# Kernel tuning notes

Hardware: AMD Instinct MI355X
Metric: run time of the kernel (lower is better)

Reference implementation:

```python
import jax, jax.numpy as jnp
import numpy as np
import math

# ---- static config (matches init_kwargs) ----
MUL = 16                       # multiplicity of 0e and 1o irreps in/out
IN_DIM = 4 * MUL               # 16x0e + 16x1o -> 16 + 48 = 64 channels
DIAMETER = 7.0
RADIUS = DIAMETER / 2.0
NRB = 8                        # num_radial_basis
STEPS = (1.0, 1.0, 1.0)
N_PATHS = 5                    # 0x0->0, 1x1->0, 0x1->1, 1x0->1, 1x1->1
WEIGHT_NUMEL = N_PATHS * MUL * MUL  # 1280


def _lattice():
    axes = []
    for st in STEPS:
        s = math.floor(RADIUS / st)
        axes.append(np.arange(-s, s + 1.0) * st)
    return np.stack(np.meshgrid(*axes, indexing='ij'), axis=-1).astype(np.float32)  # [kx,ky,kz,3]


def _radial_emb(r):
    # e3nn soft_one_hot_linspace, basis='smooth_finite', cutoff=True
    values = np.linspace(0.0, RADIUS, NRB + 2)[1:-1].astype(np.float32)
    step = values[1] - values[0]
    diff = (r[..., None] - values) / step
    def u(t):  # soft unit step: exp(-1/t) for t>0 else 0
        return np.where(t > 0.0, np.exp(-1.0 / np.where(t > 0.0, t, 1.0)), 0.0)
    return (1.14136 * math.e ** 2 * u(diff + 1.0) * u(1.0 - diff)).astype(np.float32)


def _spherical_harmonics(lat):
    # normalize=True, normalization='component': Y0 = 1, Y1 = sqrt(3) * unit_vec
    n = np.linalg.norm(lat, axis=-1, keepdims=True)
    unit = np.where(n > 0, lat / np.where(n > 0, n, 1.0), 0.0)
    return np.ones(lat.shape[:-1], np.float32), (math.sqrt(3.0) * unit).astype(np.float32)


_LAT = _lattice()
_EMB = jnp.asarray(_radial_emb(np.linalg.norm(_LAT, axis=-1)))  # [kx,ky,kz,NRB]
_sh0_np, _sh1_np = _spherical_harmonics(_LAT)
_SH0, _SH1 = jnp.asarray(_sh0_np), jnp.asarray(_sh1_np)
_eps_np = np.zeros((3, 3, 3), np.float32)
for _i, _j, _k in [(0, 1, 2), (1, 2, 0), (2, 0, 1)]:
    _eps_np[_i, _j, _k] = 1.0
    _eps_np[_i, _k, _j] = -1.0
_EPS = jnp.asarray(_eps_np)


def _build_kernel(tp_weight):
    """Radial-basis matmul + CG tensor-product -> conv kernel [out,in,kx,ky,kz]."""
    kx, ky, kz = _LAT.shape[:3]
    nk = kx * ky * kz
    w = jnp.einsum('xyzb,bn->xyzn', _EMB, tp_weight) / nk
    w = w.reshape(kx, ky, kz, N_PATHS, MUL, MUL)
    w1, w2, w3, w4, w5 = [w[..., p, :, :] for p in range(N_PATHS)]
    # e3nn path weights ('component' norm, 'element' path norm): sqrt(dim_out / fan_in)
    a0 = math.sqrt(1.0 / (2 * MUL))  # -> 0e: paths 1,2 each mul1*mul2 = MUL
    a1 = math.sqrt(3.0 / (3 * MUL))  # -> 1o: paths 3,4,5
    c1 = a0                          # w3j(0,0,0) = 1
    c2 = a0 / math.sqrt(3.0)         # w3j(1,1,0) = delta/sqrt(3)
    c3 = a1 / math.sqrt(3.0)         # w3j(0,1,1) = delta/sqrt(3)
    c4 = a1 / math.sqrt(3.0)         # w3j(1,0,1) = delta/sqrt(3)
    c5 = a1 / math.sqrt(6.0)         # w3j(1,1,1) = eps/sqrt(6)
    Kss = c1 * _SH0[..., None, None] * w1                                  # [k,u,o]
    Kvs = c2 * jnp.einsum('xyzi,xyzuo->xyzuio', _SH1, w2)                  # [k,u,3,o]
    Ksv = c3 * jnp.einsum('xyzk,xyzuo->xyzuok', _SH1, w3)                  # [k,u,o,3]
    eye3 = jnp.eye(3, dtype=w.dtype)
    Kvv = (c4 * jnp.einsum('xyz,ik,xyzuo->xyzuiok', _SH0, eye3, w4)
           + c5 * jnp.einsum('ijk,xyzj,xyzuo->xyzuiok', _EPS, _SH1, w5))   # [k,u,3,o,3]
    top = jnp.concatenate([Kss, Ksv.reshape(kx, ky, kz, MUL, 3 * MUL)], axis=-1)
    bot = jnp.concatenate([Kvs.reshape(kx, ky, kz, 3 * MUL, MUL),
                           Kvv.reshape(kx, ky, kz, 3 * MUL, 3 * MUL)], axis=-1)
    K = jnp.concatenate([top, bot], axis=-2)                               # [kx,ky,kz,in,out]
    return jnp.transpose(K, (4, 3, 0, 1, 2))                               # oixyz


def setup_inputs() -> dict:
    key = jax.random.key(0)
    k1, k2, k3, k4 = jax.random.split(key, 4)
    x = jax.random.normal(k1, (2, IN_DIM, 40, 40, 40), jnp.float32)
    sc_w0 = jax.random.normal(k2, (MUL, MUL), jnp.float32)
    sc_w1 = jax.random.normal(k3, (MUL, MUL), jnp.float32)
    tp_weight = jax.random.normal(k4, (NRB, WEIGHT_NUMEL), jnp.float32)
    return {"x": x, "sc_w0": sc_w0, "sc_w1": sc_w1, "tp_weight": tp_weight}


def reference(x, sc_w0, sc_w1, tp_weight):
    B = x.shape[0]
    sp = x.shape[2:]
    inv = 1.0 / math.sqrt(MUL)  # e3nn Linear fan-in normalization
    x0 = x[:, :MUL]                                  # [B,MUL,D,H,W]
    x1 = x[:, MUL:].reshape(B, MUL, 3, *sp)          # [B,MUL,3,D,H,W]
    sc0 = jnp.einsum('uo,budhw->bodhw', sc_w0, x0) * inv
    sc1 = jnp.einsum('uo,buidhw->boidhw', sc_w1, x1) * inv
    sc = jnp.concatenate([sc0, sc1.reshape(B, 3 * MUL, *sp)], axis=1)
    K = _build_kernel(tp_weight)
    pad = [(s // 2, s // 2) for s in K.shape[2:]]
    conv = jax.lax.conv_general_dilated(
        x, K, window_strides=(1, 1, 1), padding=pad,
        dimension_numbers=('NCDHW', 'OIDHW', 'NCDHW'))
    return sc + conv
```

## Files before the change

kernel.cpp:

```cpp
#include <hip/hip_runtime.h>
#include <stdint.h>


#define NT_REAL 179
#define NT_PAD  180
#define NPAIR   90

#define XCH  1557376
#define XCHB ((size_t)XCH * 2)

#define HBYTES 50176
#define SEGB   12288
#define NSEG   15

typedef short s16x8 __attribute__((ext_vector_type(8)));
typedef float f32x4 __attribute__((ext_vector_type(4)));
typedef float f32x16 __attribute__((ext_vector_type(16)));

struct Taps {
  int n;
  short dl16[NT_PAD];
  unsigned char dz[NT_PAD], dy[NT_PAD], dx[NT_PAD];
};
constexpr Taps mk_taps() {
  Taps t{};
  t.n = 0;
  for (int a = 0; a < 7; ++a)
    for (int b = 0; b < 7; ++b)
      for (int c = 0; c < 7; ++c) {
        int d2 = (a-3)*(a-3) + (b-3)*(b-3) + (c-3)*(c-3);
        if (d2 <= 12) {
          t.dz[t.n] = (unsigned char)a; t.dy[t.n] = (unsigned char)b;
          t.dx[t.n] = (unsigned char)c;
          t.dl16[t.n] = (short)((a*14 + b)*16 + c);
          ++t.n;
        }
      }
  for (int i = t.n; i < NT_PAD; ++i) {
    t.dz[i] = 3; t.dy[i] = 3; t.dx[i] = 3; t.dl16[i] = t.dl16[0];
  }
  return t;
}
__device__ constexpr Taps TAPS = mk_taps();
static_assert(mk_taps().n == NT_REAL, "tap count");

struct DL2 { unsigned int v[NPAIR]; };
constexpr DL2 mk_dl2() {
  DL2 d{};
  Taps t = mk_taps();
  for (int p = 0; p < NPAIR; ++p)
    d.v[p] = (unsigned int)(unsigned short)t.dl16[2*p]
           | ((unsigned int)(unsigned short)t.dl16[2*p + 1] << 16);
  return d;
}
__device__ constexpr DL2 DL2V = mk_dl2();

static __device__ inline unsigned short f2bf(float f) {
  unsigned int u = __float_as_uint(f);
  unsigned int r = u + 0x7FFFu + ((u >> 16) & 1u);
  return (unsigned short)(r >> 16);
}

__device__ __forceinline__ void gl_lds16(const void* g, void* s) {
  __builtin_amdgcn_global_load_lds(
      (const __attribute__((address_space(1))) void*)g,
      (__attribute__((address_space(3))) void*)s, 16, 0, 0);
}

__global__ void prep(const float* __restrict__ x, const float* __restrict__ scw0,
                     const float* __restrict__ scw1, const float* __restrict__ tpw,
                     unsigned short* __restrict__ Xp, unsigned short* __restrict__ Bwp) {
  __shared__ float buf[160 * 65];
  int tid = threadIdx.x;

  if (blockIdx.x < 800) {
    int blk = blockIdx.x;
    int ys = blk % 10; int t2 = blk / 10; int iz = t2 % 40; int b = t2 / 40;
    int y0 = ys * 4;
    const float* src = x + (size_t)b * 4096000 + (size_t)iz * 1600 + (size_t)y0 * 40;
    for (int e = tid; e < 64 * 160; e += 256) {
      int ch = e / 160, i = e - ch * 160;
      buf[i * 65 + ch] = src[(size_t)ch * 64000 + i];
    }
    __syncthreads();
    for (int f = tid; f < 160 * 8; f += 256) {
      int i = f >> 3, g = f & 7;
      int yy = i / 40, xx = i - yy * 40;
      s16x8 v;
      #pragma unroll
      for (int j = 0; j < 8; ++j) v[j] = (short)f2bf(buf[i * 65 + g * 8 + j]);
      size_t pos = ((size_t)((b * 46 + iz + 3) * 46 + (y0 + yy + 3)) * 46 + (xx + 3));
      *reinterpret_cast<s16x8*>(Xp + (size_t)g * XCH + pos * 8) = v;
    }
    return;
  }

  int t = blockIdx.x - 800;
  float (*wsm)[16][16] = reinterpret_cast<float (*)[16][16]>(buf);

  int dz = TAPS.dz[t], dy = TAPS.dy[t], dx = TAPS.dx[t];
  float fz = dz - 3.0f, fy = dy - 3.0f, fx = dx - 3.0f;
  float d2 = fz*fz + fy*fy + fx*fx;
  float r = sqrtf(d2);

  const float step = 3.5f / 9.0f;
  const float Cc = 1.14136f * 7.38905609893065f;
  float emb[8];
  for (int bb = 0; bb < 8; ++bb) {
    float diff = (r - step * (bb + 1)) / step;
    float t1 = diff + 1.0f, t2 = 1.0f - diff;
    float u1 = (t1 > 0.0f) ? expf(-1.0f / t1) : 0.0f;
    float u2 = (t2 > 0.0f) ? expf(-1.0f / t2) : 0.0f;
    emb[bb] = Cc * u1 * u2;
  }

  int u = tid >> 4, o = tid & 15;
  for (int p = 0; p < 5; ++p) {
    float acc = 0.0f;
    int nidx = (p * 16 + u) * 16 + o;
    for (int bb = 0; bb < 8; ++bb) acc += emb[bb] * tpw[bb * 1280 + nidx];
    wsm[p][u][o] = acc * (1.0f / 343.0f);
  }
  __syncthreads();

  float invr = (d2 > 0.0f) ? (1.7320508075688772f / r) : 0.0f;
  float sh[3] = { fz * invr, fy * invr, fx * invr };

  bool center = (dz == 3 && dy == 3 && dx == 3);
  bool padt = (t >= NT_REAL);
  const float c1 = 0.17677669529663687f;
  const float c2 = 0.10206207261596575f;
  const float c3 = 0.14433756729740643f;
  const float c4 = 0.14433756729740643f;
  const float c5 = 0.10206207261596575f;
  const float inv = 0.25f;

  for (int e = tid; e < 4096; e += 256) {
    int ich = e & 63, och = e >> 6;
    float v = 0.0f;
    if (!padt) {
      if (och < 16) {
        if (ich < 16) {
          v = c1 * wsm[0][ich][och];
          if (center) v += inv * scw0[ich * 16 + och];
        } else {
          int qq = ich - 16; int uu = qq / 3, ii = qq % 3;
          v = c2 * sh[ii] * wsm[1][uu][och];
        }
      } else {
        int qo = och - 16; int oo = qo / 3, kk = qo % 3;
        if (ich < 16) {
          v = c3 * sh[kk] * wsm[2][ich][oo];
        } else {
          int qi = ich - 16; int uu = qi / 3, ii = qi % 3;
          if (ii == kk) {
            v = c4 * wsm[3][uu][oo];
            if (center) v += inv * scw1[uu * 16 + oo];
          } else {
            int jj = 3 - ii - kk;
            float sgn = (((kk - ii + 3) % 3) == 2) ? 1.0f : -1.0f;
            v = c5 * sgn * sh[jj] * wsm[4][uu][oo];
          }
        }
      }
    }
    int chunk = ich >> 3, j = ich & 7;
    int pair = t >> 1, hi = t & 1;
    int og = och >> 5, col = och & 31;
    size_t idx = ((((size_t)chunk * NPAIR + pair) * 2 + og) * 2 + hi) * 256
               + (size_t)col * 8 + j;
    Bwp[idx] = f2bf(v);
  }
}

__global__ __launch_bounds__(256, 1) void conv3d(
    const unsigned short* __restrict__ Xp,
    const unsigned short* __restrict__ Bwp,
    float* __restrict__ out) {
  __shared__ __align__(16) unsigned char smem[2 * HBYTES + 2 * SEGB];
  unsigned char* BB = smem + 2 * HBYTES;

  int blk = blockIdx.x;
  int p = ((blk & 7) << 5) | (blk >> 3);
  if (p >= 250) return;
  int b = p / 125; int rem = p - b * 125;
  int tz = rem / 25, ty = (rem / 5) % 5, tx = rem % 5;

  int tid = threadIdx.x;
  int lane = tid & 63;
  int w = tid >> 6;
  int hi = lane >> 5, r32 = lane & 31;
  int hs = hi << 4;

  size_t hbase = (size_t)(((b * 46 + tz * 8) * 46 + ty * 8) * 46 + tx * 8) * 16;

  int abase = w * 448 + ((r32 >> 3) << 4) + (r32 & 7);

  f32x16 acc[4][2];
  #pragma unroll
  for (int f = 0; f < 4; ++f)
    #pragma unroll
    for (int og = 0; og < 2; ++og)
      #pragma unroll
      for (int e = 0; e < 16; ++e) acc[f][og][e] = 0.0f;

  auto stageB = [&](int c, int seg, unsigned char* dst) {
    const unsigned char* bg = (const unsigned char*)Bwp
        + ((size_t)c * NPAIR + seg * 6) * 2048;
    for (int k = w; k < 12; k += 4)
      gl_lds16(bg + (k << 10) + lane * 16, dst + (k << 10));
  };
  auto stageHLine = [&](int c, int k, unsigned char* dst) {
    const unsigned char* xc = (const unsigned char*)Xp + (size_t)c * XCHB + hbase;
    int sl = (k << 6) + lane;
    int hx = sl & 15; hx = hx > 13 ? 13 : hx;
    int r = sl >> 4;
    int hz = (r * 2341) >> 15;
    int hy = r - hz * 14;
    gl_lds16(xc + ((size_t)((hz * 46 + hy) * 46 + hx)) * 16, dst + (k << 10));
  };

  for (int k = w; k < 49; k += 4) stageHLine(0, k, smem);
  stageB(0, 0, BB);
  __syncthreads();

  int t = 0;
  for (int c = 0; c < 8; ++c) {
    unsigned char* XH  = smem + (c & 1) * HBYTES;
    unsigned char* XHn = smem + ((c + 1) & 1) * HBYTES;
    for (int s = 0; s < NSEG; ++s, ++t) {
      if (t + 1 < 120) {
        int cn = (s == NSEG - 1) ? c + 1 : c;
        int sn = (s == NSEG - 1) ? 0 : s + 1;
        stageB(cn, sn, BB + ((t + 1) & 1) * SEGB);
      }
      if (c + 1 < 8) {
        int L = s * 4 + w;
        if (L < 49) stageHLine(c + 1, L, XHn);
      }
      const unsigned char* BSc = BB + (t & 1) * SEGB + (size_t)lane * 16;
      #pragma unroll
      for (int pp = 0; pp < 6; ++pp) {
        unsigned int dlv = DL2V.v[s * 6 + pp];
        int dl = (int)((dlv >> hs) & 0xFFFFu);
        const unsigned char* ab = XH + ((size_t)(abase + dl) << 4);
        s16x8 a00 = *(const s16x8*)(ab);
        s16x8 a01 = *(const s16x8*)(ab + 1024);
        s16x8 a10 = *(const s16x8*)(ab + 3584);
        s16x8 a11 = *(const s16x8*)(ab + 4608);
        const unsigned char* bp = BSc + (pp << 11);
        s16x8 b0 = *(const s16x8*)(bp);
        s16x8 b1 = *(const s16x8*)(bp + 1024);
        acc[0][0] = __builtin_amdgcn_mfma_f32_32x32x16_bf16(a00, b0, acc[0][0], 0, 0, 0);
        acc[0][1] = __builtin_amdgcn_mfma_f32_32x32x16_bf16(a00, b1, acc[0][1], 0, 0, 0);
        acc[1][0] = __builtin_amdgcn_mfma_f32_32x32x16_bf16(a01, b0, acc[1][0], 0, 0, 0);
        acc[1][1] = __builtin_amdgcn_mfma_f32_32x32x16_bf16(a01, b1, acc[1][1], 0, 0, 0);
        acc[2][0] = __builtin_amdgcn_mfma_f32_32x32x16_bf16(a10, b0, acc[2][0], 0, 0, 0);
        acc[2][1] = __builtin_amdgcn_mfma_f32_32x32x16_bf16(a10, b1, acc[2][1], 0, 0, 0);
        acc[3][0] = __builtin_amdgcn_mfma_f32_32x32x16_bf16(a11, b0, acc[3][0], 0, 0, 0);
        acc[3][1] = __builtin_amdgcn_mfma_f32_32x32x16_bf16(a11, b1, acc[3][1], 0, 0, 0);
      }
      __syncthreads();
    }
  }

  int col = lane & 31;
  #pragma unroll
  for (int og = 0; og < 2; ++og) {
    #pragma unroll
    for (int f = 0; f < 4; ++f) {
      int zz = f >> 1, aq = f & 1;
      size_t cb = (size_t)(b * 64 + og * 32 + col) * 64000
                + (size_t)(tz * 8 + 2 * w + zz) * 1600
                + (size_t)(tx * 8 + hi * 4);
      #pragma unroll
      for (int ys = 0; ys < 4; ++ys) {
        float* dst = out + cb + (size_t)(ty * 8 + aq * 4 + ys) * 40;
        f32x4 v = { acc[f][og][ys * 4 + 0], acc[f][og][ys * 4 + 1],
                    acc[f][og][ys * 4 + 2], acc[f][og][ys * 4 + 3] };
        *reinterpret_cast<f32x4*>(dst) = v;
      }
    }
  }
}

extern "C" void kernel_launch(void* const* d_in, const int* in_sizes, int n_in,
                              void* d_out, int out_size, void* d_ws, size_t ws_size,
                              hipStream_t stream) {
  const float* x    = (const float*)d_in[0];
  const float* scw0 = (const float*)d_in[1];
  const float* scw1 = (const float*)d_in[2];
  const float* tpw  = (const float*)d_in[3];
  float* out = (float*)d_out;

  unsigned short* Xp  = (unsigned short*)d_ws;
  unsigned short* Bwp = Xp + (size_t)8 * XCH;

  hipMemsetAsync(Xp, 0, (size_t)8 * XCH * 2, stream);
  prep<<<800 + NT_PAD, 256, 0, stream>>>(x, scw0, scw1, tpw, Xp, Bwp);
  conv3d<<<256, 256, 0, stream>>>(Xp, Bwp, out);
}
```

Baseline: 259.5 us.

## Deepen weight-staging ring to four buffers and software-pipeline LDS fragment loads

Expands the B-weight LDS staging from a double buffer to a four-slot ring, prefetched three steps ahead. The full __syncthreads is replaced with explicit partial s_waitcnt vmcnt plus s_barrier, so global-to-LDS loads can stay in flight across steps. Inside each step, the A and B fragments for the next MFMA group are loaded into registers while the current group computes. The goal is to hide global load latency and LDS read latency behind MFMA work. The cost is extra LDS, more VGPR pressure, and hand-counted vmcnt thresholds that depend on exactly how many loads each wave issues.

```diff
diff --git a/kernel.cpp b/kernel.cpp
--- a/kernel.cpp
+++ b/kernel.cpp
@@ -12,6 +12,7 @@
 #define HBYTES 50176
 #define SEGB   12288
 #define NSEG   15
+#define NSTEP  120
 
 typedef short s16x8 __attribute__((ext_vector_type(8)));
 typedef float f32x4 __attribute__((ext_vector_type(4)));
@@ -177,7 +178,7 @@
     const unsigned short* __restrict__ Xp,
     const unsigned short* __restrict__ Bwp,
     float* __restrict__ out) {
-  __shared__ __align__(16) unsigned char smem[2 * HBYTES + 2 * SEGB];
+  __shared__ __align__(16) unsigned char smem[2 * HBYTES + 4 * SEGB];
   unsigned char* BB = smem + 2 * HBYTES;
 
   int blk = blockIdx.x;
@@ -204,9 +205,11 @@
       #pragma unroll
       for (int e = 0; e < 16; ++e) acc[f][og][e] = 0.0f;
 
-  auto stageB = [&](int c, int seg, unsigned char* dst) {
+  auto stageB = [&](int st) {
+    int cn = st / NSEG, sn = st - cn * NSEG;
     const unsigned char* bg = (const unsigned char*)Bwp
-        + ((size_t)c * NPAIR + seg * 6) * 2048;
+        + ((size_t)cn * NPAIR + sn * 6) * 2048;
+    unsigned char* dst = BB + (size_t)(st & 3) * SEGB;
     for (int k = w; k < 12; k += 4)
       gl_lds16(bg + (k << 10) + lane * 16, dst + (k << 10));
   };
@@ -221,46 +224,63 @@
   };
 
   for (int k = w; k < 49; k += 4) stageHLine(0, k, smem);
-  stageB(0, 0, BB);
-  __syncthreads();
+  stageB(0); stageB(1); stageB(2);
+  asm volatile("s_waitcnt vmcnt(6)" ::: "memory");
+  __builtin_amdgcn_s_barrier();
 
   int t = 0;
   for (int c = 0; c < 8; ++c) {
     unsigned char* XH  = smem + (c & 1) * HBYTES;
     unsigned char* XHn = smem + ((c + 1) & 1) * HBYTES;
     for (int s = 0; s < NSEG; ++s, ++t) {
-      if (t + 1 < 120) {
-        int cn = (s == NSEG - 1) ? c + 1 : c;
-        int sn = (s == NSEG - 1) ? 0 : s + 1;
-        stageB(cn, sn, BB + ((t + 1) & 1) * SEGB);
-      }
+      if (t + 3 < NSTEP) stageB(t + 3);
       if (c + 1 < 8) {
         int L = s * 4 + w;
         if (L < 49) stageHLine(c + 1, L, XHn);
       }
-      const unsigned char* BSc = BB + (t & 1) * SEGB + (size_t)lane * 16;
+
+      const unsigned char* BSc = BB + (size_t)(t & 3) * SEGB + (size_t)lane * 16;
+      s16x8 fa[2][4], fb[2][2];
+      {
+        unsigned int dlv = DL2V.v[s * 6];
+        int dl = (int)((dlv >> hs) & 0xFFFFu);
+        const unsigned char* ab = XH + ((size_t)(abase + dl) << 4);
+        fa[0][0] = *(const s16x8*)(ab);
+        fa[0][1] = *(const s16x8*)(ab + 1024);
+        fa[0][2] = *(const s16x8*)(ab + 3584);
+        fa[0][3] = *(const s16x8*)(ab + 4608);
+        fb[0][0] = *(const s16x8*)(BSc);
+        fb[0][1] = *(const s16x8*)(BSc + 1024);
+      }
       #pragma unroll
       for (int pp = 0; pp < 6; ++pp) {
-        unsigned int dlv = DL2V.v[s * 6 + pp];
-        int dl = (int)((dlv >> hs) & 0xFFFFu);
-        const unsigned char* ab = XH + ((size_t)(abase + dl) << 4);
-        s16x8 a00 = *(const s16x8*)(ab);
-        s16x8 a01 = *(const s16x8*)(ab + 1024);
-        s16x8 a10 = *(const s16x8*)(ab + 3584);
-        s16x8 a11 = *(const s16x8*)(ab + 4608);
-        const unsigned char* bp = BSc + (pp << 11);
-        s16x8 b0 = *(const s16x8*)(bp);
-        s16x8 b1 = *(const s16x8*)(bp + 1024);
-        acc[0][0] = __builtin_amdgcn_mfma_f32_32x32x16_bf16(a00, b0, acc[0][0], 0, 0, 0);
-        acc[0][1] = __builtin_amdgcn_mfma_f32_32x32x16_bf16(a00, b1, acc[0][1], 0, 0, 0);
-        acc[1][0] = __builtin_amdgcn_mfma_f32_32x32x16_bf16(a01, b0, acc[1][0], 0, 0, 0);
-        acc[1][1] = __builtin_amdgcn_mfma_f32_32x32x16_bf16(a01, b1, acc[1][1], 0, 0, 0);
-        acc[2][0] = __builtin_amdgcn_mfma_f32_32x32x16_bf16(a10, b0, acc[2][0], 0, 0, 0);
-        acc[2][1] = __builtin_amdgcn_mfma_f32_32x32x16_bf16(a10, b1, acc[2][1], 0, 0, 0);
-        acc[3][0] = __builtin_amdgcn_mfma_f32_32x32x16_bf16(a11, b0, acc[3][0], 0, 0, 0);
-        acc[3][1] = __builtin_amdgcn_mfma_f32_32x32x16_bf16(a11, b1, acc[3][1], 0, 0, 0);
-      }
-      __syncthreads();
+        int cur = pp & 1, nxt = cur ^ 1;
+        if (pp < 5) {
+          unsigned int dlv = DL2V.v[s * 6 + pp + 1];
+          int dl = (int)((dlv >> hs) & 0xFFFFu);
+          const unsigned char* ab = XH + ((size_t)(abase + dl) << 4);
+          fa[nxt][0] = *(const s16x8*)(ab);
+          fa[nxt][1] = *(const s16x8*)(ab + 1024);
+          fa[nxt][2] = *(const s16x8*)(ab + 3584);
+          fa[nxt][3] = *(const s16x8*)(ab + 4608);
+          const unsigned char* bp = BSc + ((pp + 1) << 11);
+          fb[nxt][0] = *(const s16x8*)(bp);
+          fb[nxt][1] = *(const s16x8*)(bp + 1024);
+        }
+        acc[0][0] = __builtin_amdgcn_mfma_f32_32x32x16_bf16(fa[cur][0], fb[cur][0], acc[0][0], 0, 0, 0);
+        acc[0][1] = __builtin_amdgcn_mfma_f32_32x32x16_bf16(fa[cur][0], fb[cur][1], acc[0][1], 0, 0, 0);
+        acc[1][0] = __builtin_amdgcn_mfma_f32_32x32x16_bf16(fa[cur][1], fb[cur][0], acc[1][0], 0, 0, 0);
+        acc[1][1] = __builtin_amdgcn_mfma_f32_32x32x16_bf16(fa[cur][1], fb[cur][1], acc[1][1], 0, 0, 0);
+        acc[2][0] = __builtin_amdgcn_mfma_f32_32x32x16_bf16(fa[cur][2], fb[cur][0], acc[2][0], 0, 0, 0);
+        acc[2][1] = __builtin_amdgcn_mfma_f32_32x32x16_bf16(fa[cur][2], fb[cur][1], acc[2][1], 0, 0, 0);
+        acc[3][0] = __builtin_amdgcn_mfma_f32_32x32x16_bf16(fa[cur][3], fb[cur][0], acc[3][0], 0, 0, 0);
+        acc[3][1] = __builtin_amdgcn_mfma_f32_32x32x16_bf16(fa[cur][3], fb[cur][1], acc[3][1], 0, 0, 0);
+      }
+
+      if (t <= NSTEP - 4)      asm volatile("s_waitcnt vmcnt(6)" ::: "memory");
+      else if (t == NSTEP - 3) asm volatile("s_waitcnt vmcnt(3)" ::: "memory");
+      else                     asm volatile("s_waitcnt vmcnt(0)" ::: "memory");
+      __builtin_amdgcn_s_barrier();
     }
   }
 
```

Measured after the change: 264.4 us. Within noise of the previous version (+1.9%).
